# Optimization experiments

Hardware: AMD Instinct MI355X
Metric: run time of the kernel (lower is better)

Reference implementation:

```python
import jax, jax.numpy as jnp
import numpy as np

EPS = 1e-6

def rms_norm(x):
    return x * jax.lax.rsqrt(jnp.mean(x * x, axis=-1, keepdims=True) + EPS)

def setup_inputs() -> dict:
    key = jax.random.key(0)
    k_x, k_w = jax.random.split(key)
    T, B, D = 2048, 16, 1024
    x = jax.random.normal(k_x, (T, B, D), dtype=jnp.float32)
    h0 = jnp.zeros((B, D), dtype=jnp.float32)
    # xavier_uniform for W: limit = sqrt(6/(fan_in+fan_out)) = sqrt(6/(2D))
    limit = float(np.sqrt(6.0 / (2 * D)))
    W = jax.random.uniform(k_w, (D, D), dtype=jnp.float32, minval=-limit, maxval=limit)
    b = jnp.zeros((D,), dtype=jnp.float32)
    log_alpha = jnp.asarray(np.log(0.1), dtype=jnp.float32)
    return {"x": x, "h0": h0, "W": W, "b": b, "log_alpha": log_alpha}

def reference(x, h0, W, b, log_alpha):
    # x: [T,B,D], h0: [B,D], W: [D,D], b: [D], log_alpha: []
    alpha = jnp.exp(log_alpha)
    # Precompute all input projections in one big GEMM: [T,B,D]
    Wx_all = jnp.einsum('tbd,ed->tbe', x, W) + b

    def step(h, wx):
        h_new = rms_norm(h + alpha * wx)
        out = h_new * jax.nn.silu(h_new)
        return h_new, (h_new, out)

    _, (hs, outs) = jax.lax.scan(step, h0, Wx_all)
    h = jnp.concatenate([h0[None], hs], axis=0)  # [T+1,B,D]
    return outs, h
```

## Files before the change

kernel.cpp:

```cpp
#include <hip/hip_runtime.h>
#include <hip/hip_bf16.h>

#define T_STEPS 2048
#define BATCH 16
#define DIM 1024
#define EPSV 1e-6f
#define INVD (1.0f / 1024.0f)
#define SLOTF (BATCH * DIM)
#define SLOT4C (BATCH * DIM / 4)

typedef short short8 __attribute__((ext_vector_type(8)));
typedef float f32x4 __attribute__((ext_vector_type(4)));

struct alignas(16) bf16x8pack { __hip_bfloat16 v[8]; };

__device__ __forceinline__ float dot4(const float4& a, const float4& c) {
  return fmaf(a.x, c.x, fmaf(a.y, c.y, fmaf(a.z, c.z, a.w * c.w)));
}

__global__ __launch_bounds__(256) void cvt_kernel(const float* __restrict__ src,
                                                  bf16x8pack* __restrict__ dst, int n8) {
  int i = blockIdx.x * blockDim.x + threadIdx.x;
  if (i >= n8) return;
  const float4* s4 = (const float4*)src + (size_t)i * 2;
  float4 a = s4[0];
  float4 b = s4[1];
  bf16x8pack p;
  p.v[0] = __float2bfloat16(a.x); p.v[1] = __float2bfloat16(a.y);
  p.v[2] = __float2bfloat16(a.z); p.v[3] = __float2bfloat16(a.w);
  p.v[4] = __float2bfloat16(b.x); p.v[5] = __float2bfloat16(b.y);
  p.v[6] = __float2bfloat16(b.z); p.v[7] = __float2bfloat16(b.w);
  dst[i] = p;
}

__global__ __launch_bounds__(256) void gemm_kernel(
    const __hip_bfloat16* __restrict__ Xb,
    const __hip_bfloat16* __restrict__ Wb,
    const float* __restrict__ bias,
    const float* __restrict__ log_alpha_p,
    float* __restrict__ hreg) {
  __shared__ __hip_bfloat16 As[128 * 32];
  __shared__ __hip_bfloat16 Bs[128 * 32];
  const int tid = threadIdx.x;
  const int wave = tid >> 6, lane = tid & 63;
  const int m0 = blockIdx.y * 128;
  const int e0 = blockIdx.x * 128;
  const int wm = (wave >> 1) * 64;
  const int wn = (wave & 1) * 64;
  const int l15 = lane & 15, l4 = lane >> 4;

  f32x4 acc[4][4] = {};

  const int srow = wave * 16 + (lane >> 2);
  const int sch = (lane & 3) * 8;

  for (int kt = 0; kt < DIM; kt += 32) {
    __syncthreads();
#pragma unroll
    for (int i = 0; i < 2; ++i) {
      const __hip_bfloat16* ga = Xb + (size_t)(m0 + i * 64 + srow) * DIM + kt + sch;
      const __hip_bfloat16* gb = Wb + (size_t)(e0 + i * 64 + srow) * DIM + kt + sch;
      __builtin_amdgcn_global_load_lds(
          (const __attribute__((address_space(1))) void*)ga,
          (__attribute__((address_space(3))) void*)((char*)As + (i * 64 + wave * 16) * 64),
          16, 0, 0);
      __builtin_amdgcn_global_load_lds(
          (const __attribute__((address_space(1))) void*)gb,
          (__attribute__((address_space(3))) void*)((char*)Bs + (i * 64 + wave * 16) * 64),
          16, 0, 0);
    }
    __syncthreads();
    short8 a[4], b[4];
#pragma unroll
    for (int f = 0; f < 4; ++f)
      a[f] = *(const short8*)((const char*)As + ((wm + f * 16 + l15) * 32 + l4 * 8) * 2);
#pragma unroll
    for (int g = 0; g < 4; ++g)
      b[g] = *(const short8*)((const char*)Bs + ((wn + g * 16 + l15) * 32 + l4 * 8) * 2);
#pragma unroll
    for (int f = 0; f < 4; ++f)
#pragma unroll
      for (int g = 0; g < 4; ++g)
        acc[f][g] = __builtin_amdgcn_mfma_f32_16x16x32_bf16(a[f], b[g], acc[f][g], 0, 0, 0);
  }
  const float alpha = __expf(log_alpha_p[0]);
#pragma unroll
  for (int g = 0; g < 4; ++g) {
    const int e = e0 + wn + g * 16 + l15;
    const float bv = bias[e];
#pragma unroll
    for (int f = 0; f < 4; ++f) {
#pragma unroll
      for (int r = 0; r < 4; ++r) {
        const int m = m0 + wm + f * 16 + l4 * 4 + r;
        hreg[(size_t)(m + BATCH) * DIM + e] = alpha * (acc[f][g][r] + bv);
      }
    }
  }
}

__device__ __forceinline__ float dpp_sum_reg(float x) {
  float acc = x;
#define DPP_ADD(ctrl)                                                              \
  {                                                                                \
    int t_ = __builtin_amdgcn_update_dpp(0, __float_as_int(acc), (ctrl), 0xf, 0xf, \
                                         true);                                    \
    acc += __int_as_float(t_);                                                     \
  }
  DPP_ADD(0x111); DPP_ADD(0x112); DPP_ADD(0x114); DPP_ADD(0x118);
  DPP_ADD(0x142); DPP_ADD(0x143);
#undef DPP_ADD
  return acc;
}

__global__ __launch_bounds__(64) void dots_kernel(const float* __restrict__ hreg,
                                                  float4* __restrict__ scal4,
                                                  float* __restrict__ d4g) {
  const int t = blockIdx.x >> 4;
  const int b = blockIdx.x & 15;
  const int lane = threadIdx.x;
  const float4* w  = (const float4*)(hreg + (size_t)(t + 1) * SLOTF + b * DIM);
  const float4* m1 = (const float4*)(hreg + (size_t)(t    ) * SLOTF + b * DIM);
  const float4* m2 = (const float4*)(hreg + (size_t)(t - 1) * SLOTF + b * DIM);
  const float4* m3 = (const float4*)(hreg + (size_t)(t - 2) * SLOTF + b * DIM);
  const float4* m4 = (const float4*)(hreg + (size_t)(t - 3) * SLOTF + b * DIM);
  float e = 0.f, d = 0.f, d2 = 0.f, d3 = 0.f, d4 = 0.f;
#pragma unroll
  for (int j = 0; j < 4; ++j) {
    float4 a = w[lane + 64 * j];
    e = fmaf(a.x, a.x, fmaf(a.y, a.y, fmaf(a.z, a.z, fmaf(a.w, a.w, e))));
    if (t >= 1) { float4 p = m1[lane + 64 * j];
      d = fmaf(p.x, a.x, fmaf(p.y, a.y, fmaf(p.z, a.z, fmaf(p.w, a.w, d)))); }
    if (t >= 2) { float4 p = m2[lane + 64 * j];
      d2 = fmaf(p.x, a.x, fmaf(p.y, a.y, fmaf(p.z, a.z, fmaf(p.w, a.w, d2)))); }
    if (t >= 3) { float4 p = m3[lane + 64 * j];
      d3 = fmaf(p.x, a.x, fmaf(p.y, a.y, fmaf(p.z, a.z, fmaf(p.w, a.w, d3)))); }
    if (t >= 4) { float4 p = m4[lane + 64 * j];
      d4 = fmaf(p.x, a.x, fmaf(p.y, a.y, fmaf(p.z, a.z, fmaf(p.w, a.w, d4)))); }
  }
  e = dpp_sum_reg(e);
  d = dpp_sum_reg(d);
  d2 = dpp_sum_reg(d2);
  d3 = dpp_sum_reg(d3);
  d4 = dpp_sum_reg(d4);
  if (lane == 63) {
    scal4[b * T_STEPS + t] = make_float4(e, d + d, d2 + d2, d3 + d3);
    d4g[b * T_STEPS + t] = d4 + d4;
  }
}

__global__ __launch_bounds__(256) void scan_kernel(
    const float* __restrict__ h0,
    const float4* __restrict__ scal4,
    const float* __restrict__ d4g,
    float* __restrict__ hreg) {
  const int b = blockIdx.x;
  const int tid = threadIdx.x;
  const int wave = tid >> 6;
  const int lane = tid & 63;
  float4* h4 = (float4*)hreg;
  const int idx4 = b * 256 + tid;

  __shared__ float4 scLDS[T_STEPS];
  __shared__ float d4LDS[T_STEPS];
  __shared__ alignas(16) float Gp[4][4];
  __shared__ float initP[4][8];

#pragma unroll
  for (int p = 0; p < 8; ++p)
    scLDS[p * 256 + tid] = scal4[b * T_STEPS + p * 256 + tid];
#pragma unroll
  for (int p = 0; p < 8; ++p)
    d4LDS[p * 256 + tid] = d4g[b * T_STEPS + p * 256 + tid];

  float4 w[8];
  w[2] = h4[(size_t)SLOT4C * 3 + idx4];
  w[3] = h4[(size_t)SLOT4C * 4 + idx4];
  w[4] = h4[(size_t)SLOT4C * 5 + idx4];
  w[5] = h4[(size_t)SLOT4C * 6 + idx4];
  w[6] = h4[(size_t)SLOT4C * 7 + idx4];
  w[7] = h4[(size_t)SLOT4C * 8 + idx4];
  w[0] = h4[(size_t)SLOT4C * 9 + idx4];
  w[1] = h4[(size_t)SLOT4C * 10 + idx4];
  float4 w0v = h4[(size_t)SLOT4C * 1 + idx4];
  float4 w1v = h4[(size_t)SLOT4C * 2 + idx4];
  float4 h0v = ((const float4*)h0)[idx4];
  h4[idx4] = h0v;

  float4 s;
  s.x = h0v.x + w0v.x; s.y = h0v.y + w0v.y;
  s.z = h0v.z + w0v.z; s.w = h0v.w + w0v.w;
  float q = dpp_sum_reg(dot4(s, s));
  float r = dpp_sum_reg(dot4(s, w1v));
  float u2 = dpp_sum_reg(dot4(s, w[2]));
  float u3 = dpp_sum_reg(dot4(s, w[3]));
  float g4 = dpp_sum_reg(dot4(h0v, w[4]));
  if (lane == 63) {
    initP[wave][0] = q; initP[wave][1] = r; initP[wave][2] = u2;
    initP[wave][3] = g4; initP[wave][4] = u3;
  }
  __syncthreads();
  const float n1 = (initP[0][0] + initP[1][0]) + (initP[2][0] + initP[3][0]);
  float bs = (initP[0][1] + initP[1][1]) + (initP[2][1] + initP[3][1]);
  float c2s = (initP[0][2] + initP[1][2]) + (initP[2][2] + initP[3][2]);
  float g4s = (initP[0][3] + initP[1][3]) + (initP[2][3] + initP[3][3]);
  float c3s = (initP[0][4] + initP[1][4]) + (initP[2][4] + initP[3][4]);
  const float B1 = bs + bs;
  const float C2 = c2s + c2s;
  const float C3 = c3s + c3s;
  float gr0 = g4s + g4s;
  float gr1 = 0.0f;

  const float e1 = scLDS[1].x;
  float4 sc2 = scLDS[2], sc3 = scLDS[3];
  float4 scA = scLDS[4], scB = scLDS[5];
  float d4A = d4LDS[4], d4B = d4LDS[5];
  float4 rv = make_float4(0.f, 0.f, 0.f, 0.f);
  float n = n1, rm1, rm2, rm3, pp;

  {
    const float rinv = rsqrtf(fmaf(n, INVD, EPSV));
    n = fmaf(rinv, fmaf(rinv, n, B1), e1);
    float4 hv;
    hv.x = rinv * s.x; hv.y = rinv * s.y; hv.z = rinv * s.z; hv.w = rinv * s.w;
    h4[(size_t)SLOT4C * 1 + idx4] = hv;
    s.x = hv.x + w1v.x; s.y = hv.y + w1v.y; s.z = hv.z + w1v.z; s.w = hv.w + w1v.w;
    pp = dpp_sum_reg(dot4(hv, w[5]));
    rm1 = rinv;
    asm volatile("s_waitcnt lgkmcnt(0)" ::: "memory");
    __builtin_amdgcn_s_barrier();
  }
  {
    if (lane == 63) Gp[1][wave] = pp;
    const float rinv = rsqrtf(fmaf(n, INVD, EPSV));
    const float BB = fmaf(rm1, C2, sc2.y);
    n = fmaf(rinv, fmaf(rinv, n, BB), sc2.x);
    float4 hv;
    hv.x = rinv * s.x; hv.y = rinv * s.y; hv.z = rinv * s.z; hv.w = rinv * s.w;
    h4[(size_t)SLOT4C * 2 + idx4] = hv;
    s.x = hv.x + w[2].x; s.y = hv.y + w[2].y; s.z = hv.z + w[2].z; s.w = hv.w + w[2].w;
    pp = dpp_sum_reg(dot4(hv, w[6]));
    w[2] = h4[(size_t)SLOT4C * 11 + idx4];
    rm2 = rm1; rm1 = rinv;
    asm volatile("s_waitcnt lgkmcnt(0)" ::: "memory");
    __builtin_amdgcn_s_barrier();
  }
  {
    if (lane == 63) Gp[2][wave] = pp;
    const float rinv = rsqrtf(fmaf(n, INVD, EPSV));
    const float BB = fmaf(rm1, fmaf(rm2, C3, sc3.z), sc3.y);
    n = fmaf(rinv, fmaf(rinv, n, BB), sc3.x);
    rv = *(const float4*)&Gp[1][0];
    float4 hv;
    hv.x = rinv * s.x; hv.y = rinv * s.y; hv.z = rinv * s.z; hv.w = rinv * s.w;
    h4[(size_t)SLOT4C * 3 + idx4] = hv;
    s.x = hv.x + w[3].x; s.y = hv.y + w[3].y; s.z = hv.z + w[3].z; s.w = hv.w + w[3].w;
    pp = dpp_sum_reg(dot4(hv, w[7]));
    w[3] = h4[(size_t)SLOT4C * 12 + idx4];
    rm3 = rm2; rm2 = rm1; rm1 = rinv;
    asm volatile("s_waitcnt lgkmcnt(0)" ::: "memory");
    __builtin_amdgcn_s_barrier();
  }

#define STEP(I_, WS, W4S, GW, GR, SC, D4R, GRU, GRW)                                 \
  {                                                                                  \
    const int i_ = (I_);                                                             \
    if (lane == 63) Gp[GW][wave] = pp;                                               \
    asm volatile("" ::: "memory");                                                   \
    const float rinv = rsqrtf(fmaf(n, INVD, EPSV));                                  \
    const float BB =                                                                 \
        fmaf(rm1, fmaf(rm2, fmaf(rm3, (D4R) + (GRU), (SC).w), (SC).z), (SC).y);      \
    n = fmaf(rinv, fmaf(rinv, n, BB), (SC).x);                                       \
    {                                                                                \
      float gt_ = (rv.x + rv.y) + (rv.z + rv.w);                                     \
      GRW = gt_ + gt_;                                                               \
    }                                                                                \
    rv = *(const float4*)&Gp[GR][0];                                                 \
    const int isc_ = (i_ + 2 < T_STEPS) ? (i_ + 2) : (T_STEPS - 1);                  \
    SC = scLDS[isc_];                                                                \
    D4R = d4LDS[isc_];                                                               \
    float4 hv_;                                                                      \
    hv_.x = rinv * s.x; hv_.y = rinv * s.y;                                          \
    hv_.z = rinv * s.z; hv_.w = rinv * s.w;                                          \
    h4[(size_t)SLOT4C * i_ + idx4] = hv_;                                            \
    s.x = hv_.x + w[WS].x; s.y = hv_.y + w[WS].y;                                    \
    s.z = hv_.z + w[WS].z; s.w = hv_.w + w[WS].w;                                    \
    pp = dpp_sum_reg(dot4(hv_, w[W4S]));                                             \
    const int ipf_ = (i_ + 8 < T_STEPS) ? (i_ + 8) : (T_STEPS - 1);                  \
    w[WS] = h4[(size_t)SLOT4C * (ipf_ + 1) + idx4];                                  \
    rm3 = rm2; rm2 = rm1; rm1 = rinv;                                                \
    asm volatile("s_waitcnt lgkmcnt(3)" ::: "memory");                               \
    __builtin_amdgcn_s_barrier();                                                    \
  }

  for (int ii = 4; ii <= 2036; ii += 8) {
    STEP(ii + 0, 4, 0, 3, 2, scA, d4A, gr0, gr1)
    STEP(ii + 1, 5, 1, 0, 3, scB, d4B, gr1, gr0)
    STEP(ii + 2, 6, 2, 1, 0, scA, d4A, gr0, gr1)
    STEP(ii + 3, 7, 3, 2, 1, scB, d4B, gr1, gr0)
    STEP(ii + 4, 0, 4, 3, 2, scA, d4A, gr0, gr1)
    STEP(ii + 5, 1, 5, 0, 3, scB, d4B, gr1, gr0)
    STEP(ii + 6, 2, 6, 1, 0, scA, d4A, gr0, gr1)
    STEP(ii + 7, 3, 7, 2, 1, scB, d4B, gr1, gr0)
  }
  STEP(2044, 4, 0, 3, 2, scA, d4A, gr0, gr1)
  STEP(2045, 5, 1, 0, 3, scB, d4B, gr1, gr0)
  STEP(2046, 6, 2, 1, 0, scA, d4A, gr0, gr1)
  STEP(2047, 7, 3, 2, 1, scB, d4B, gr1, gr0)
#undef STEP

  const float rinvT = rsqrtf(fmaf(n, INVD, EPSV));
  float4 o;
  o.x = rinvT * s.x; o.y = rinvT * s.y; o.z = rinvT * s.z; o.w = rinvT * s.w;
  h4[(size_t)SLOT4C * T_STEPS + idx4] = o;
}

__global__ __launch_bounds__(256) void silu_kernel(const float4* __restrict__ hsrc,
                                                   float4* __restrict__ out4, int n4) {
  int i = blockIdx.x * blockDim.x + threadIdx.x;
  if (i >= n4) return;
  float4 h = hsrc[i];
  float4 o;
  o.x = h.x * h.x / (1.f + __expf(-h.x));
  o.y = h.y * h.y / (1.f + __expf(-h.y));
  o.z = h.z * h.z / (1.f + __expf(-h.z));
  o.w = h.w * h.w / (1.f + __expf(-h.w));
  out4[i] = o;
}

extern "C" void kernel_launch(void* const* d_in, const int* in_sizes, int n_in,
                              void* d_out, int out_size, void* d_ws, size_t ws_size,
                              hipStream_t stream) {
  (void)in_sizes; (void)n_in; (void)d_ws; (void)ws_size; (void)out_size;
  const float* x = (const float*)d_in[0];
  const float* h0 = (const float*)d_in[1];
  const float* W = (const float*)d_in[2];
  const float* bias = (const float*)d_in[3];
  const float* log_alpha = (const float*)d_in[4];

  float* out = (float*)d_out;
  float* hreg = out + (size_t)T_STEPS * BATCH * DIM;
  __hip_bfloat16* xb = (__hip_bfloat16*)d_out;
  __hip_bfloat16* wb = (__hip_bfloat16*)((char*)d_out + (size_t)T_STEPS * BATCH * DIM * 2);
  float4* scal4 = (float4*)(out + (size_t)26 * 1024 * 1024);
  float* d4g = out + (size_t)27 * 1024 * 1024;

  const int nx8 = T_STEPS * BATCH * DIM / 8;
  const int nw8 = DIM * DIM / 8;
  cvt_kernel<<<nx8 / 256, 256, 0, stream>>>(x, (bf16x8pack*)xb, nx8);
  cvt_kernel<<<nw8 / 256, 256, 0, stream>>>(W, (bf16x8pack*)wb, nw8);

  dim3 ggrid(DIM / 128, (T_STEPS * BATCH) / 128);
  gemm_kernel<<<ggrid, 256, 0, stream>>>(xb, wb, bias, log_alpha, hreg);

  dots_kernel<<<T_STEPS * BATCH, 64, 0, stream>>>(hreg, scal4, d4g);

  scan_kernel<<<BATCH, 256, 0, stream>>>(h0, scal4, d4g, hreg);

  const int n4 = T_STEPS * BATCH * DIM / 4;
  silu_kernel<<<n4 / 256, 256, 0, stream>>>((const float4*)(hreg + BATCH * DIM),
                                            (float4*)out, n4);
}
```

Before: 592.4 us.

## Deepen scan lookahead to five lags, barrier every other step, use raw rsq

Extends the precomputed dot-product lag window from four to five steps, so the cross-wave partial reduction can be consumed two steps later and a workgroup barrier is needed only on every other step. The register prefetch window for future inputs doubles from 8 to 16 slots, and rsqrtf is replaced with the raw v_rsq_f32 instruction. This targets the per-step serial latency of the 2048-step scan. In exchange the dots kernel does extra reads and FMAs, register pressure in the scan rises, and the approximate rsq may change numerics slightly.

```diff
diff --git a/kernel.cpp b/kernel.cpp
--- a/kernel.cpp
+++ b/kernel.cpp
@@ -16,6 +16,12 @@
 
 __device__ __forceinline__ float dot4(const float4& a, const float4& c) {
   return fmaf(a.x, c.x, fmaf(a.y, c.y, fmaf(a.z, c.z, a.w * c.w)));
+}
+
+__device__ __forceinline__ float fast_rsq(float x) {
+  float r;
+  asm("v_rsq_f32 %0, %1" : "=v"(r) : "v"(x));
+  return r;
 }
 
 __global__ __launch_bounds__(256) void cvt_kernel(const float* __restrict__ src,
@@ -115,7 +121,7 @@
 
 __global__ __launch_bounds__(64) void dots_kernel(const float* __restrict__ hreg,
                                                   float4* __restrict__ scal4,
-                                                  float* __restrict__ d4g) {
+                                                  float2* __restrict__ d45g) {
   const int t = blockIdx.x >> 4;
   const int b = blockIdx.x & 15;
   const int lane = threadIdx.x;
@@ -124,7 +130,8 @@
   const float4* m2 = (const float4*)(hreg + (size_t)(t - 1) * SLOTF + b * DIM);
   const float4* m3 = (const float4*)(hreg + (size_t)(t - 2) * SLOTF + b * DIM);
   const float4* m4 = (const float4*)(hreg + (size_t)(t - 3) * SLOTF + b * DIM);
-  float e = 0.f, d = 0.f, d2 = 0.f, d3 = 0.f, d4 = 0.f;
+  const float4* m5 = (const float4*)(hreg + (size_t)(t - 4) * SLOTF + b * DIM);
+  float e = 0.f, d = 0.f, d2 = 0.f, d3 = 0.f, d4 = 0.f, d5 = 0.f;
 #pragma unroll
   for (int j = 0; j < 4; ++j) {
     float4 a = w[lane + 64 * j];
@@ -137,22 +144,25 @@
       d3 = fmaf(p.x, a.x, fmaf(p.y, a.y, fmaf(p.z, a.z, fmaf(p.w, a.w, d3)))); }
     if (t >= 4) { float4 p = m4[lane + 64 * j];
       d4 = fmaf(p.x, a.x, fmaf(p.y, a.y, fmaf(p.z, a.z, fmaf(p.w, a.w, d4)))); }
+    if (t >= 5) { float4 p = m5[lane + 64 * j];
+      d5 = fmaf(p.x, a.x, fmaf(p.y, a.y, fmaf(p.z, a.z, fmaf(p.w, a.w, d5)))); }
   }
   e = dpp_sum_reg(e);
   d = dpp_sum_reg(d);
   d2 = dpp_sum_reg(d2);
   d3 = dpp_sum_reg(d3);
   d4 = dpp_sum_reg(d4);
+  d5 = dpp_sum_reg(d5);
   if (lane == 63) {
     scal4[b * T_STEPS + t] = make_float4(e, d + d, d2 + d2, d3 + d3);
-    d4g[b * T_STEPS + t] = d4 + d4;
-  }
-}
-
-__global__ __launch_bounds__(256) void scan_kernel(
+    d45g[b * T_STEPS + t] = make_float2(d4 + d4, d5 + d5);
+  }
+}
+
+__global__ __launch_bounds__(256, 1) void scan_kernel(
     const float* __restrict__ h0,
     const float4* __restrict__ scal4,
-    const float* __restrict__ d4g,
+    const float2* __restrict__ d45g,
     float* __restrict__ hreg) {
   const int b = blockIdx.x;
   const int tid = threadIdx.x;
@@ -162,26 +172,22 @@
   const int idx4 = b * 256 + tid;
 
   __shared__ float4 scLDS[T_STEPS];
-  __shared__ float d4LDS[T_STEPS];
+  __shared__ float2 d45LDS[T_STEPS];
   __shared__ alignas(16) float Gp[4][4];
-  __shared__ float initP[4][8];
+  __shared__ float initP[4][6];
 
 #pragma unroll
   for (int p = 0; p < 8; ++p)
     scLDS[p * 256 + tid] = scal4[b * T_STEPS + p * 256 + tid];
 #pragma unroll
   for (int p = 0; p < 8; ++p)
-    d4LDS[p * 256 + tid] = d4g[b * T_STEPS + p * 256 + tid];
-
-  float4 w[8];
-  w[2] = h4[(size_t)SLOT4C * 3 + idx4];
-  w[3] = h4[(size_t)SLOT4C * 4 + idx4];
-  w[4] = h4[(size_t)SLOT4C * 5 + idx4];
-  w[5] = h4[(size_t)SLOT4C * 6 + idx4];
-  w[6] = h4[(size_t)SLOT4C * 7 + idx4];
-  w[7] = h4[(size_t)SLOT4C * 8 + idx4];
-  w[0] = h4[(size_t)SLOT4C * 9 + idx4];
-  w[1] = h4[(size_t)SLOT4C * 10 + idx4];
+    d45LDS[p * 256 + tid] = d45g[b * T_STEPS + p * 256 + tid];
+
+  float4 w[16];
+#pragma unroll
+  for (int k = 2; k < 16; ++k) w[k] = h4[(size_t)SLOT4C * (k + 1) + idx4];
+  w[0] = h4[(size_t)SLOT4C * 17 + idx4];
+  w[1] = h4[(size_t)SLOT4C * 18 + idx4];
   float4 w0v = h4[(size_t)SLOT4C * 1 + idx4];
   float4 w1v = h4[(size_t)SLOT4C * 2 + idx4];
   float4 h0v = ((const float4*)h0)[idx4];
@@ -190,126 +196,170 @@
   float4 s;
   s.x = h0v.x + w0v.x; s.y = h0v.y + w0v.y;
   s.z = h0v.z + w0v.z; s.w = h0v.w + w0v.w;
-  float q = dpp_sum_reg(dot4(s, s));
-  float r = dpp_sum_reg(dot4(s, w1v));
-  float u2 = dpp_sum_reg(dot4(s, w[2]));
-  float u3 = dpp_sum_reg(dot4(s, w[3]));
-  float g4 = dpp_sum_reg(dot4(h0v, w[4]));
-  if (lane == 63) {
-    initP[wave][0] = q; initP[wave][1] = r; initP[wave][2] = u2;
-    initP[wave][3] = g4; initP[wave][4] = u3;
+  {
+    float q  = dpp_sum_reg(dot4(s, s));
+    float r  = dpp_sum_reg(dot4(s, w1v));
+    float c2 = dpp_sum_reg(dot4(s, w[2]));
+    float c3 = dpp_sum_reg(dot4(s, w[3]));
+    float c4 = dpp_sum_reg(dot4(s, w[4]));
+    float c5 = dpp_sum_reg(dot4(s, w[5]));
+    if (lane == 63) {
+      initP[wave][0] = q;  initP[wave][1] = r;  initP[wave][2] = c2;
+      initP[wave][3] = c3; initP[wave][4] = c4; initP[wave][5] = c5;
+    }
   }
   __syncthreads();
   const float n1 = (initP[0][0] + initP[1][0]) + (initP[2][0] + initP[3][0]);
-  float bs = (initP[0][1] + initP[1][1]) + (initP[2][1] + initP[3][1]);
-  float c2s = (initP[0][2] + initP[1][2]) + (initP[2][2] + initP[3][2]);
-  float g4s = (initP[0][3] + initP[1][3]) + (initP[2][3] + initP[3][3]);
-  float c3s = (initP[0][4] + initP[1][4]) + (initP[2][4] + initP[3][4]);
-  const float B1 = bs + bs;
-  const float C2 = c2s + c2s;
-  const float C3 = c3s + c3s;
-  float gr0 = g4s + g4s;
-  float gr1 = 0.0f;
+  float t1 = (initP[0][1] + initP[1][1]) + (initP[2][1] + initP[3][1]);
+  float t2 = (initP[0][2] + initP[1][2]) + (initP[2][2] + initP[3][2]);
+  float t3 = (initP[0][3] + initP[1][3]) + (initP[2][3] + initP[3][3]);
+  float t4 = (initP[0][4] + initP[1][4]) + (initP[2][4] + initP[3][4]);
+  float t5 = (initP[0][5] + initP[1][5]) + (initP[2][5] + initP[3][5]);
+  const float B1 = t1 + t1, C2 = t2 + t2, C3 = t3 + t3, C4 = t4 + t4, C5 = t5 + t5;
 
   const float e1 = scLDS[1].x;
-  float4 sc2 = scLDS[2], sc3 = scLDS[3];
-  float4 scA = scLDS[4], scB = scLDS[5];
-  float d4A = d4LDS[4], d4B = d4LDS[5];
+  float4 sc2 = scLDS[2], sc3 = scLDS[3], sc4 = scLDS[4], sc5 = scLDS[5];
+  const float D45x = d45LDS[5].x;
+  float4 scA = scLDS[6], scB = scLDS[7];
+  float2 d45A = d45LDS[6], d45B = d45LDS[7];
+
+  float n = n1, rm1, rm2, rm3, rm4, pp;
+  float gr0 = 0.f, gr1 = 0.f;
   float4 rv = make_float4(0.f, 0.f, 0.f, 0.f);
-  float n = n1, rm1, rm2, rm3, pp;
-
-  {
-    const float rinv = rsqrtf(fmaf(n, INVD, EPSV));
+
+#define BAR1 { asm volatile("s_waitcnt lgkmcnt(0)" ::: "memory"); __builtin_amdgcn_s_barrier(); }
+
+  {
+    const float rinv = fast_rsq(fmaf(n, INVD, EPSV));
     n = fmaf(rinv, fmaf(rinv, n, B1), e1);
     float4 hv;
     hv.x = rinv * s.x; hv.y = rinv * s.y; hv.z = rinv * s.z; hv.w = rinv * s.w;
     h4[(size_t)SLOT4C * 1 + idx4] = hv;
     s.x = hv.x + w1v.x; s.y = hv.y + w1v.y; s.z = hv.z + w1v.z; s.w = hv.w + w1v.w;
-    pp = dpp_sum_reg(dot4(hv, w[5]));
+    pp = dpp_sum_reg(dot4(hv, w[6]));
     rm1 = rinv;
-    asm volatile("s_waitcnt lgkmcnt(0)" ::: "memory");
-    __builtin_amdgcn_s_barrier();
-  }
-  {
-    if (lane == 63) Gp[1][wave] = pp;
-    const float rinv = rsqrtf(fmaf(n, INVD, EPSV));
+    BAR1
+  }
+  {
+    if (lane == 63) Gp[2][wave] = pp;
+    const float rinv = fast_rsq(fmaf(n, INVD, EPSV));
     const float BB = fmaf(rm1, C2, sc2.y);
     n = fmaf(rinv, fmaf(rinv, n, BB), sc2.x);
     float4 hv;
     hv.x = rinv * s.x; hv.y = rinv * s.y; hv.z = rinv * s.z; hv.w = rinv * s.w;
     h4[(size_t)SLOT4C * 2 + idx4] = hv;
     s.x = hv.x + w[2].x; s.y = hv.y + w[2].y; s.z = hv.z + w[2].z; s.w = hv.w + w[2].w;
-    pp = dpp_sum_reg(dot4(hv, w[6]));
-    w[2] = h4[(size_t)SLOT4C * 11 + idx4];
+    pp = dpp_sum_reg(dot4(hv, w[7]));
+    w[2] = h4[(size_t)SLOT4C * 19 + idx4];
     rm2 = rm1; rm1 = rinv;
-    asm volatile("s_waitcnt lgkmcnt(0)" ::: "memory");
-    __builtin_amdgcn_s_barrier();
-  }
-  {
-    if (lane == 63) Gp[2][wave] = pp;
-    const float rinv = rsqrtf(fmaf(n, INVD, EPSV));
+    BAR1
+  }
+  {
+    if (lane == 63) Gp[3][wave] = pp;
+    const float rinv = fast_rsq(fmaf(n, INVD, EPSV));
     const float BB = fmaf(rm1, fmaf(rm2, C3, sc3.z), sc3.y);
     n = fmaf(rinv, fmaf(rinv, n, BB), sc3.x);
-    rv = *(const float4*)&Gp[1][0];
     float4 hv;
     hv.x = rinv * s.x; hv.y = rinv * s.y; hv.z = rinv * s.z; hv.w = rinv * s.w;
     h4[(size_t)SLOT4C * 3 + idx4] = hv;
     s.x = hv.x + w[3].x; s.y = hv.y + w[3].y; s.z = hv.z + w[3].z; s.w = hv.w + w[3].w;
-    pp = dpp_sum_reg(dot4(hv, w[7]));
-    w[3] = h4[(size_t)SLOT4C * 12 + idx4];
+    pp = dpp_sum_reg(dot4(hv, w[8]));
+    w[3] = h4[(size_t)SLOT4C * 20 + idx4];
     rm3 = rm2; rm2 = rm1; rm1 = rinv;
-    asm volatile("s_waitcnt lgkmcnt(0)" ::: "memory");
-    __builtin_amdgcn_s_barrier();
-  }
-
-#define STEP(I_, WS, W4S, GW, GR, SC, D4R, GRU, GRW)                                 \
+    BAR1
+  }
+  {
+    if (lane == 63) Gp[0][wave] = pp;
+    const float rinv = fast_rsq(fmaf(n, INVD, EPSV));
+    const float BB = fmaf(rm1, fmaf(rm2, fmaf(rm3, C4, sc4.w), sc4.z), sc4.y);
+    n = fmaf(rinv, fmaf(rinv, n, BB), sc4.x);
+    rv = *(const float4*)&Gp[2][0];
+    float4 hv;
+    hv.x = rinv * s.x; hv.y = rinv * s.y; hv.z = rinv * s.z; hv.w = rinv * s.w;
+    h4[(size_t)SLOT4C * 4 + idx4] = hv;
+    s.x = hv.x + w[4].x; s.y = hv.y + w[4].y; s.z = hv.z + w[4].z; s.w = hv.w + w[4].w;
+    pp = dpp_sum_reg(dot4(hv, w[9]));
+    w[4] = h4[(size_t)SLOT4C * 21 + idx4];
+    rm4 = rm3; rm3 = rm2; rm2 = rm1; rm1 = rinv;
+    BAR1
+  }
+  {
+    if (lane == 63) Gp[1][wave] = pp;
+    const float rinv = fast_rsq(fmaf(n, INVD, EPSV));
+    const float BB =
+        fmaf(rm1, fmaf(rm2, fmaf(rm3, fmaf(rm4, C5, D45x), sc5.w), sc5.z), sc5.y);
+    n = fmaf(rinv, fmaf(rinv, n, BB), sc5.x);
+    { float gt = (rv.x + rv.y) + (rv.z + rv.w); gr0 = gt + gt; }
+    rv = *(const float4*)&Gp[3][0];
+    float4 hv;
+    hv.x = rinv * s.x; hv.y = rinv * s.y; hv.z = rinv * s.z; hv.w = rinv * s.w;
+    h4[(size_t)SLOT4C * 5 + idx4] = hv;
+    s.x = hv.x + w[5].x; s.y = hv.y + w[5].y; s.z = hv.z + w[5].z; s.w = hv.w + w[5].w;
+    pp = dpp_sum_reg(dot4(hv, w[10]));
+    w[5] = h4[(size_t)SLOT4C * 22 + idx4];
+    rm4 = rm3; rm3 = rm2; rm2 = rm1; rm1 = rinv;
+    BAR1
+  }
+
+#define STEP(I_, WS, W5S, GW, GR, SCR, D45R, GRU, GRW, BAR_)                         \
   {                                                                                  \
     const int i_ = (I_);                                                             \
     if (lane == 63) Gp[GW][wave] = pp;                                               \
-    asm volatile("" ::: "memory");                                                   \
-    const float rinv = rsqrtf(fmaf(n, INVD, EPSV));                                  \
-    const float BB =                                                                 \
-        fmaf(rm1, fmaf(rm2, fmaf(rm3, (D4R) + (GRU), (SC).w), (SC).z), (SC).y);      \
-    n = fmaf(rinv, fmaf(rinv, n, BB), (SC).x);                                       \
-    {                                                                                \
-      float gt_ = (rv.x + rv.y) + (rv.z + rv.w);                                     \
-      GRW = gt_ + gt_;                                                               \
-    }                                                                                \
+    const float rinv = fast_rsq(fmaf(n, INVD, EPSV));                                \
+    const float BB = fmaf(                                                           \
+        rm1, fmaf(rm2, fmaf(rm3, fmaf(rm4, (D45R).y + (GRU), (D45R).x), (SCR).w),    \
+                  (SCR).z), (SCR).y);                                                \
+    n = fmaf(rinv, fmaf(rinv, n, BB), (SCR).x);                                      \
+    { float gt_ = (rv.x + rv.y) + (rv.z + rv.w); GRW = gt_ + gt_; }                  \
     rv = *(const float4*)&Gp[GR][0];                                                 \
-    const int isc_ = (i_ + 2 < T_STEPS) ? (i_ + 2) : (T_STEPS - 1);                  \
-    SC = scLDS[isc_];                                                                \
-    D4R = d4LDS[isc_];                                                               \
     float4 hv_;                                                                      \
     hv_.x = rinv * s.x; hv_.y = rinv * s.y;                                          \
     hv_.z = rinv * s.z; hv_.w = rinv * s.w;                                          \
     h4[(size_t)SLOT4C * i_ + idx4] = hv_;                                            \
     s.x = hv_.x + w[WS].x; s.y = hv_.y + w[WS].y;                                    \
     s.z = hv_.z + w[WS].z; s.w = hv_.w + w[WS].w;                                    \
-    pp = dpp_sum_reg(dot4(hv_, w[W4S]));                                             \
-    const int ipf_ = (i_ + 8 < T_STEPS) ? (i_ + 8) : (T_STEPS - 1);                  \
+    pp = dpp_sum_reg(dot4(hv_, w[W5S]));                                             \
+    const int ipf_ = (i_ + 16 < T_STEPS) ? (i_ + 16) : (T_STEPS - 1);                \
     w[WS] = h4[(size_t)SLOT4C * (ipf_ + 1) + idx4];                                  \
-    rm3 = rm2; rm2 = rm1; rm1 = rinv;                                                \
-    asm volatile("s_waitcnt lgkmcnt(3)" ::: "memory");                               \
-    __builtin_amdgcn_s_barrier();                                                    \
-  }
-
-  for (int ii = 4; ii <= 2036; ii += 8) {
-    STEP(ii + 0, 4, 0, 3, 2, scA, d4A, gr0, gr1)
-    STEP(ii + 1, 5, 1, 0, 3, scB, d4B, gr1, gr0)
-    STEP(ii + 2, 6, 2, 1, 0, scA, d4A, gr0, gr1)
-    STEP(ii + 3, 7, 3, 2, 1, scB, d4B, gr1, gr0)
-    STEP(ii + 4, 0, 4, 3, 2, scA, d4A, gr0, gr1)
-    STEP(ii + 5, 1, 5, 0, 3, scB, d4B, gr1, gr0)
-    STEP(ii + 6, 2, 6, 1, 0, scA, d4A, gr0, gr1)
-    STEP(ii + 7, 3, 7, 2, 1, scB, d4B, gr1, gr0)
-  }
-  STEP(2044, 4, 0, 3, 2, scA, d4A, gr0, gr1)
-  STEP(2045, 5, 1, 0, 3, scB, d4B, gr1, gr0)
-  STEP(2046, 6, 2, 1, 0, scA, d4A, gr0, gr1)
-  STEP(2047, 7, 3, 2, 1, scB, d4B, gr1, gr0)
+    const int isc_ = (i_ + 2 < T_STEPS) ? (i_ + 2) : (T_STEPS - 1);                  \
+    SCR = scLDS[isc_];                                                               \
+    D45R = d45LDS[isc_];                                                             \
+    rm4 = rm3; rm3 = rm2; rm2 = rm1; rm1 = rinv;                                     \
+    if (BAR_) BAR1                                                                   \
+  }
+
+  for (int ii = 6; ii < 2038; ii += 16) {
+    STEP(ii + 0,  6, 11, 2, 0, scA, d45A, gr0, gr1, 0)
+    STEP(ii + 1,  7, 12, 3, 1, scB, d45B, gr1, gr0, 1)
+    STEP(ii + 2,  8, 13, 0, 2, scA, d45A, gr0, gr1, 0)
+    STEP(ii + 3,  9, 14, 1, 3, scB, d45B, gr1, gr0, 1)
+    STEP(ii + 4, 10, 15, 2, 0, scA, d45A, gr0, gr1, 0)
+    STEP(ii + 5, 11,  0, 3, 1, scB, d45B, gr1, gr0, 1)
+    STEP(ii + 6, 12,  1, 0, 2, scA, d45A, gr0, gr1, 0)
+    STEP(ii + 7, 13,  2, 1, 3, scB, d45B, gr1, gr0, 1)
+    STEP(ii + 8, 14,  3, 2, 0, scA, d45A, gr0, gr1, 0)
+    STEP(ii + 9, 15,  4, 3, 1, scB, d45B, gr1, gr0, 1)
+    STEP(ii + 10, 0,  5, 0, 2, scA, d45A, gr0, gr1, 0)
+    STEP(ii + 11, 1,  6, 1, 3, scB, d45B, gr1, gr0, 1)
+    STEP(ii + 12, 2,  7, 2, 0, scA, d45A, gr0, gr1, 0)
+    STEP(ii + 13, 3,  8, 3, 1, scB, d45B, gr1, gr0, 1)
+    STEP(ii + 14, 4,  9, 0, 2, scA, d45A, gr0, gr1, 0)
+    STEP(ii + 15, 5, 10, 1, 3, scB, d45B, gr1, gr0, 1)
+  }
+  STEP(2038,  6, 11, 2, 0, scA, d45A, gr0, gr1, 0)
+  STEP(2039,  7, 12, 3, 1, scB, d45B, gr1, gr0, 1)
+  STEP(2040,  8, 13, 0, 2, scA, d45A, gr0, gr1, 0)
+  STEP(2041,  9, 14, 1, 3, scB, d45B, gr1, gr0, 1)
+  STEP(2042, 10, 15, 2, 0, scA, d45A, gr0, gr1, 0)
+  STEP(2043, 11,  0, 3, 1, scB, d45B, gr1, gr0, 1)
+  STEP(2044, 12,  1, 0, 2, scA, d45A, gr0, gr1, 0)
+  STEP(2045, 13,  2, 1, 3, scB, d45B, gr1, gr0, 1)
+  STEP(2046, 14,  3, 2, 0, scA, d45A, gr0, gr1, 0)
+  STEP(2047, 15,  4, 3, 1, scB, d45B, gr1, gr0, 1)
 #undef STEP
-
-  const float rinvT = rsqrtf(fmaf(n, INVD, EPSV));
+#undef BAR1
+
+  const float rinvT = fast_rsq(fmaf(n, INVD, EPSV));
   float4 o;
   o.x = rinvT * s.x; o.y = rinvT * s.y; o.z = rinvT * s.z; o.w = rinvT * s.w;
   h4[(size_t)SLOT4C * T_STEPS + idx4] = o;
@@ -343,7 +393,7 @@
   __hip_bfloat16* xb = (__hip_bfloat16*)d_out;
   __hip_bfloat16* wb = (__hip_bfloat16*)((char*)d_out + (size_t)T_STEPS * BATCH * DIM * 2);
   float4* scal4 = (float4*)(out + (size_t)26 * 1024 * 1024);
-  float* d4g = out + (size_t)27 * 1024 * 1024;
+  float2* d45g = (float2*)(out + (size_t)27 * 1024 * 1024);
 
   const int nx8 = T_STEPS * BATCH * DIM / 8;
   const int nw8 = DIM * DIM / 8;
@@ -353,9 +403,9 @@
   dim3 ggrid(DIM / 128, (T_STEPS * BATCH) / 128);
   gemm_kernel<<<ggrid, 256, 0, stream>>>(xb, wb, bias, log_alpha, hreg);
 
-  dots_kernel<<<T_STEPS * BATCH, 64, 0, stream>>>(hreg, scal4, d4g);
-
-  scan_kernel<<<BATCH, 256, 0, stream>>>(h0, scal4, d4g, hreg);
+  dots_kernel<<<T_STEPS * BATCH, 64, 0, stream>>>(hreg, scal4, d45g);
+
+  scan_kernel<<<BATCH, 256, 0, stream>>>(h0, scal4, d45g, hreg);
 
   const int n4 = T_STEPS * BATCH * DIM / 4;
   silu_kernel<<<n4 / 256, 256, 0, stream>>>((const float4*)(hreg + BATCH * DIM),
```

New measurement: 553.0 us. 1.07x faster.
